# Performance work log

Hardware: AMD Instinct MI355X
Metric: run time of the kernel (lower is better)

The kernel has to match this reference:

```python
import jax, jax.numpy as jnp
import numpy as np

K = 1e-3          # sigmoid temperature from MAPLoss(k=0.001): sigmoid(x) = 1/(1+exp(-x/K))
N, D = 512, 128   # batch of embeddings
NUM_CLASSES = 32
EPS = 1e-8


def setup_inputs() -> dict:
    key = jax.random.key(0)
    k1, k2 = jax.random.split(key)
    return {
        "input": jax.random.normal(k1, (N, D), dtype=jnp.float32),
        "target": jax.random.randint(k2, (N,), 0, NUM_CLASSES, dtype=jnp.int64),
    }


def _offdiag_cols(n):
    # cols[i, j] = j-th column index != i, in increasing order (matches
    # torch sm[~eye].view(n, n-1) row-major off-diagonal extraction)
    idx = jnp.arange(n - 1)[None, :]
    rows = jnp.arange(n)[:, None]
    return idx + (idx >= rows)  # [n, n-1] int


def reference(input, target):
    n = input.shape[0]
    # cosine similarity matrix
    norms = jnp.maximum(jnp.linalg.norm(input, axis=1, keepdims=True), EPS)
    xn = input / norms
    sm = xn @ xn.T  # [n, n]

    cols = _offdiag_cols(n)  # [n, n-1]
    ranking = jnp.take_along_axis(sm, cols, axis=1)  # [n, n-1]
    gt_full = (target[None, :] == target[:, None])    # [n, n] bool
    gt = jnp.take_along_axis(gt_full, cols, axis=1).astype(input.dtype)  # [n, n-1]

    # indicator[i, j, l] = sigmoid((r[i, l] - r[i, j]) / K)   -- O(n^3) cube
    indicator = jax.nn.sigmoid((ranking[:, None, :] - ranking[:, :, None]) / K)

    accumulated_gt = jnp.einsum('il,ijl->ij', gt, indicator)  # [n, n-1]
    denom = indicator.sum(-1) + 0.5                           # [n, n-1]
    prec = accumulated_gt / denom
    ap = jnp.sum(gt * prec, axis=1)    # [n]
    num_positives = gt.sum(-1)         # [n]

    valid = num_positives > 0
    ap_norm = jnp.where(valid, ap / jnp.where(valid, num_positives, 1.0), 0.0)
    n_valid = valid.sum().astype(input.dtype)
    return 1.0 - ap_norm.sum() / n_valid
```

## Files before the change

### kernel.cpp

```cpp
#include <hip/hip_runtime.h>

#define N 512
#define D 128
#define TS 32
#define RS_SCALE 1442.6950408889634f
#define W_INV (1.0f / 18.0f)
#define B_OFF 1530.0f
#define PADV -1600.0f
#define NB 172

static __device__ __forceinline__ float rcp_fast(float x) {
    return __builtin_amdgcn_rcpf(x);
}
static __device__ __forceinline__ float exp2_fast(float x) {
    return __builtin_amdgcn_exp2f(x);
}

__global__ __launch_bounds__(256) void map_sim_kernel(
    const float* __restrict__ x, float* __restrict__ rs,
    int* __restrict__ ticket)
{
    const int bi = blockIdx.x, bj = blockIdx.y, t = threadIdx.x;
    __shared__ float As[TS * D], Bs[TS * D];
    __shared__ float ssA[TS], ssB[TS];
    __shared__ float invA[TS], invB[TS];

    if (bi == 0 && bj == 0 && t == 0) *ticket = 0;

    const int lane = t & 63;
#pragma unroll
    for (int r = 0; r < 4; ++r) {
        int ch = t + 256 * r;
        int row = ch >> 5, c4 = ch & 31;
        int sw = (c4 ^ (row >> 1)) << 2;
        float4 va = *(const float4*)(x + (bi * TS + row) * D + c4 * 4);
        *(float4*)(As + row * D + sw) = va;
        float pa = va.x * va.x + va.y * va.y + va.z * va.z + va.w * va.w;
        float4 vb = *(const float4*)(x + (bj * TS + row) * D + c4 * 4);
        *(float4*)(Bs + row * D + sw) = vb;
        float pb = vb.x * vb.x + vb.y * vb.y + vb.z * vb.z + vb.w * vb.w;
#pragma unroll
        for (int off = 16; off; off >>= 1) {
            pa += __shfl_xor(pa, off);
            pb += __shfl_xor(pb, off);
        }
        if ((lane & 31) == 0) { ssA[row] = pa; ssB[row] = pb; }
    }
    __syncthreads();
    if (t < TS)          invA[t] = rcp_fast(fmaxf(sqrtf(ssA[t]), 1e-8f));
    else if (t < 2 * TS) invB[t - TS] = rcp_fast(fmaxf(sqrtf(ssB[t - TS]), 1e-8f));
    __syncthreads();

    const int tx = t & 15, ty = t >> 4;
    float acc00 = 0.f, acc01 = 0.f, acc10 = 0.f, acc11 = 0.f;
#pragma unroll 4
    for (int k4 = 0; k4 < D / 4; ++k4) {
        float4 a0 = *(const float4*)(As + (2 * ty) * D + ((k4 ^ ty) << 2));
        float4 a1 = *(const float4*)(As + (2 * ty + 1) * D + ((k4 ^ ty) << 2));
        float4 b0 = *(const float4*)(Bs + (2 * tx) * D + ((k4 ^ tx) << 2));
        float4 b1 = *(const float4*)(Bs + (2 * tx + 1) * D + ((k4 ^ tx) << 2));
        acc00 = fmaf(a0.x, b0.x, acc00); acc00 = fmaf(a0.y, b0.y, acc00);
        acc00 = fmaf(a0.z, b0.z, acc00); acc00 = fmaf(a0.w, b0.w, acc00);
        acc01 = fmaf(a0.x, b1.x, acc01); acc01 = fmaf(a0.y, b1.y, acc01);
        acc01 = fmaf(a0.z, b1.z, acc01); acc01 = fmaf(a0.w, b1.w, acc01);
        acc10 = fmaf(a1.x, b0.x, acc10); acc10 = fmaf(a1.y, b0.y, acc10);
        acc10 = fmaf(a1.z, b0.z, acc10); acc10 = fmaf(a1.w, b0.w, acc10);
        acc11 = fmaf(a1.x, b1.x, acc11); acc11 = fmaf(a1.y, b1.y, acc11);
        acc11 = fmaf(a1.z, b1.z, acc11); acc11 = fmaf(a1.w, b1.w, acc11);
    }

    const float sA0 = invA[2 * ty] * RS_SCALE;
    const float sA1 = invA[2 * ty + 1] * RS_SCALE;
    const float sB0 = invB[2 * tx], sB1 = invB[2 * tx + 1];
    const int gr = bi * TS + 2 * ty, gc = bj * TS + 2 * tx;
    *(float2*)(rs + gr * N + gc) =
        make_float2(acc00 * sA0 * sB0, acc01 * sA0 * sB1);
    *(float2*)(rs + (gr + 1) * N + gc) =
        make_float2(acc10 * sA1 * sB0, acc11 * sA1 * sB1);
}

__global__ __launch_bounds__(256) void map_ap_kernel(
    const float* __restrict__ rs, const int* __restrict__ tgt,
    float2* __restrict__ av, int* __restrict__ ticket,
    float* __restrict__ out)
{
    const int i = blockIdx.x, t = threadIdx.x;
    const int lane = t & 63;
    __shared__ int hist[256];
    __shared__ int offs[NB];
    __shared__ int wtot[4];
    __shared__ __align__(16) float2 skv[N];
    __shared__ float red[8];
    __shared__ int amLast;

    hist[t] = 0;
    if (t < NB) offs[t] = 0;
    const int ti = tgt[i];
    float val[2]; int gti[2], q[2];
#pragma unroll
    for (int e = 0; e < 2; ++e) {
        int c = t + 256 * e;
        bool self = (c == i);
        val[e] = self ? PADV : rs[i * N + c];
        gti[e] = (!self && tgt[c] == ti) ? 1 : 0;
        int qq = (int)((val[e] + B_OFF) * W_INV);
        q[e] = max(0, min(NB - 1, qq));
    }
    __syncthreads();
    atomicAdd(&hist[q[0]], (1 << 10) | gti[0]);
    atomicAdd(&hist[q[1]], (1 << 10) | gti[1]);
    __syncthreads();

    int v = hist[t];
#pragma unroll
    for (int off = 1; off < 64; off <<= 1) {
        int u = __shfl_up(v, off);
        if (lane >= off) v += u;
    }
    if (lane == 63) wtot[t >> 6] = v;
    __syncthreads();
    {
        int w = t >> 6, add = 0;
        if (w > 0) add += wtot[0];
        if (w > 1) add += wtot[1];
        if (w > 2) add += wtot[2];
        hist[t] = v + add;
    }
    __syncthreads();

#pragma unroll
    for (int e = 0; e < 2; ++e) {
        int base = (q[e] > 0) ? (hist[q[e] - 1] >> 10) : 0;
        int pos = base + atomicAdd(&offs[q[e]], 1);
        skv[pos] = make_float2(val[e], (float)gti[e]);
    }
    __syncthreads();

    const int totGt = hist[NB - 1] & 1023;
    const float4* skv4 = (const float4*)skv;

    float apAcc = 0.f, npAcc = 0.f;
#pragma unroll
    for (int ri = 0; ri < 2; ++ri) {
        const int p = t + 256 * ri;
        const float2 me = skv[p];
        const float rj = me.x, gtj = me.y;
        int qj = (int)((rj + B_OFF) * W_INV);
        qj = max(0, min(NB - 1, qj));
        const int qlo = __shfl(qj, 0);
        const int qhi = __shfl(qj, 63);
        const int lo = (qlo > 1) ? (hist[qlo - 2] >> 10) : 0;
        const int e1 = min(qhi + 1, NB - 1);
        const int hi = hist[e1] >> 10;

        float dsum = (float)(N - hi);
        float gsum = (float)(totGt - (hist[e1] & 1023));
        int k = lo & ~1;
        for (; k + 2 <= hi; k += 2) {
            float4 kv = skv4[k >> 1];
            float s0 = rcp_fast(1.f + exp2_fast(rj - kv.x));
            float s1 = rcp_fast(1.f + exp2_fast(rj - kv.z));
            dsum += s0 + s1;
            gsum = fmaf(kv.y, s0, gsum);
            gsum = fmaf(kv.w, s1, gsum);
        }
        if (k < hi) {
            float2 kv = skv[k];
            float s = rcp_fast(1.f + exp2_fast(rj - kv.x));
            dsum += s;
            gsum = fmaf(kv.y, s, gsum);
        }
        apAcc += gtj * gsum * rcp_fast(dsum + 0.5f);
        npAcc += gtj;
    }

#pragma unroll
    for (int off = 32; off; off >>= 1) {
        apAcc += __shfl_down(apAcc, off);
        npAcc += __shfl_down(npAcc, off);
    }
    if (lane == 0) { red[(t >> 6) * 2] = apAcc; red[(t >> 6) * 2 + 1] = npAcc; }
    __syncthreads();
    if (t == 0) {
        float A = red[0] + red[2] + red[4] + red[6];
        float P = red[1] + red[3] + red[5] + red[7];
        av[i] = make_float2((P > 0.f) ? (A * rcp_fast(P)) : 0.f,
                            (P > 0.f) ? 1.f : 0.f);
        __threadfence();
        int old = atomicAdd(ticket, 1);
        amLast = (old == (int)gridDim.x - 1) ? 1 : 0;
    }
    __syncthreads();

    if (amLast) {
        __threadfence();
        float2 p0 = av[t], p1 = av[t + 256];
        float a = p0.x + p1.x, vv = p0.y + p1.y;
#pragma unroll
        for (int off = 32; off; off >>= 1) {
            a += __shfl_down(a, off);
            vv += __shfl_down(vv, off);
        }
        if (lane == 0) { red[(t >> 6) * 2] = a; red[(t >> 6) * 2 + 1] = vv; }
        __syncthreads();
        if (t == 0) {
            float A = red[0] + red[2] + red[4] + red[6];
            float V = red[1] + red[3] + red[5] + red[7];
            out[0] = 1.0f - A * rcp_fast(V);
        }
    }
}

extern "C" void kernel_launch(void* const* d_in, const int* in_sizes, int n_in,
                              void* d_out, int out_size, void* d_ws, size_t ws_size,
                              hipStream_t stream) {
    const float* x = (const float*)d_in[0];
    const int* tgt = (const int*)d_in[1];
    float* out = (float*)d_out;

    float* rs = (float*)d_ws;
    float2* av = (float2*)((char*)d_ws + N * N * 4);
    int* ticket = (int*)((char*)d_ws + N * N * 4 + N * 8);

    map_sim_kernel<<<dim3(N / TS, N / TS), 256, 0, stream>>>(x, rs, ticket);
    map_ap_kernel<<<N, 256, 0, stream>>>(rs, tgt, av, ticket, out);
}
```

Baseline: 33.01 us.

## Pack ground-truth flags into bitmask and unroll sigmoid window loop by eight

Replaces the interleaved (value, gt) float2 shared array with a separate float key array and a 512-bit gt bitmask built with atomicOr. The windowed sigmoid loop now handles eight keys per iteration with two float4 loads and one bitmask word, spreading the sums over four independent accumulators to expose ILP. The global loads of rs and tgt are also hoisted ahead of the shared-memory initialisation. This halves shared-memory traffic for the keys, in exchange for extra bit-extract and select instructions, an atomicOr pass during the scatter, and a scalar tail loop that can run longer because the start is aligned down to a multiple of eight.

```diff
diff --git a/kernel.cpp b/kernel.cpp
--- a/kernel.cpp
+++ b/kernel.cpp
@@ -89,20 +89,27 @@
     __shared__ int hist[256];
     __shared__ int offs[NB];
     __shared__ int wtot[4];
-    __shared__ __align__(16) float2 skv[N];
+    __shared__ unsigned gbits[16];
+    __shared__ __align__(16) float skey[N];
     __shared__ float red[8];
     __shared__ int amLast;
 
+    const int ti = tgt[i];
+    const float v0raw = rs[i * N + t];
+    const float v1raw = rs[i * N + t + 256];
+    const int tg0 = tgt[t], tg1 = tgt[t + 256];
+
     hist[t] = 0;
     if (t < NB) offs[t] = 0;
-    const int ti = tgt[i];
+    if (t < 16) gbits[t] = 0u;
+
     float val[2]; int gti[2], q[2];
+    val[0] = (t == i) ? PADV : v0raw;
+    val[1] = (t + 256 == i) ? PADV : v1raw;
+    gti[0] = (t != i && tg0 == ti) ? 1 : 0;
+    gti[1] = (t + 256 != i && tg1 == ti) ? 1 : 0;
 #pragma unroll
     for (int e = 0; e < 2; ++e) {
-        int c = t + 256 * e;
-        bool self = (c == i);
-        val[e] = self ? PADV : rs[i * N + c];
-        gti[e] = (!self && tgt[c] == ti) ? 1 : 0;
         int qq = (int)((val[e] + B_OFF) * W_INV);
         q[e] = max(0, min(NB - 1, qq));
     }
@@ -132,19 +139,20 @@
     for (int e = 0; e < 2; ++e) {
         int base = (q[e] > 0) ? (hist[q[e] - 1] >> 10) : 0;
         int pos = base + atomicAdd(&offs[q[e]], 1);
-        skv[pos] = make_float2(val[e], (float)gti[e]);
+        skey[pos] = val[e];
+        if (gti[e]) atomicOr(&gbits[pos >> 5], 1u << (pos & 31));
     }
     __syncthreads();
 
     const int totGt = hist[NB - 1] & 1023;
-    const float4* skv4 = (const float4*)skv;
+    const float4* sk4 = (const float4*)skey;
 
     float apAcc = 0.f, npAcc = 0.f;
 #pragma unroll
     for (int ri = 0; ri < 2; ++ri) {
         const int p = t + 256 * ri;
-        const float2 me = skv[p];
-        const float rj = me.x, gtj = me.y;
+        const float rj = skey[p];
+        const float gtj = (float)((gbits[p >> 5] >> (p & 31)) & 1u);
         int qj = (int)((rj + B_OFF) * W_INV);
         qj = max(0, min(NB - 1, qj));
         const int qlo = __shfl(qj, 0);
@@ -155,21 +163,40 @@
 
         float dsum = (float)(N - hi);
         float gsum = (float)(totGt - (hist[e1] & 1023));
-        int k = lo & ~1;
-        for (; k + 2 <= hi; k += 2) {
-            float4 kv = skv4[k >> 1];
-            float s0 = rcp_fast(1.f + exp2_fast(rj - kv.x));
-            float s1 = rcp_fast(1.f + exp2_fast(rj - kv.z));
-            dsum += s0 + s1;
-            gsum = fmaf(kv.y, s0, gsum);
-            gsum = fmaf(kv.w, s1, gsum);
-        }
-        if (k < hi) {
-            float2 kv = skv[k];
-            float s = rcp_fast(1.f + exp2_fast(rj - kv.x));
+
+        float d0 = 0.f, d1 = 0.f, d2 = 0.f, d3 = 0.f;
+        float g0 = 0.f, g1 = 0.f, g2 = 0.f, g3 = 0.f;
+        int k = lo & ~7;
+        for (; k + 8 <= hi; k += 8) {
+            float4 ka = sk4[k >> 2];
+            float4 kb = sk4[(k >> 2) + 1];
+            unsigned gw = (gbits[k >> 5] >> (k & 31)) & 0xffu;
+            float s0 = rcp_fast(1.f + exp2_fast(rj - ka.x));
+            float s1 = rcp_fast(1.f + exp2_fast(rj - ka.y));
+            float s2 = rcp_fast(1.f + exp2_fast(rj - ka.z));
+            float s3 = rcp_fast(1.f + exp2_fast(rj - ka.w));
+            float s4 = rcp_fast(1.f + exp2_fast(rj - kb.x));
+            float s5 = rcp_fast(1.f + exp2_fast(rj - kb.y));
+            float s6 = rcp_fast(1.f + exp2_fast(rj - kb.z));
+            float s7 = rcp_fast(1.f + exp2_fast(rj - kb.w));
+            d0 += s0 + s4; d1 += s1 + s5; d2 += s2 + s6; d3 += s3 + s7;
+            g0 += ((gw      ) & 1u) ? s0 : 0.f;
+            g1 += ((gw >> 1u) & 1u) ? s1 : 0.f;
+            g2 += ((gw >> 2u) & 1u) ? s2 : 0.f;
+            g3 += ((gw >> 3u) & 1u) ? s3 : 0.f;
+            g0 += ((gw >> 4u) & 1u) ? s4 : 0.f;
+            g1 += ((gw >> 5u) & 1u) ? s5 : 0.f;
+            g2 += ((gw >> 6u) & 1u) ? s6 : 0.f;
+            g3 += ((gw >> 7u) & 1u) ? s7 : 0.f;
+        }
+        dsum += (d0 + d1) + (d2 + d3);
+        gsum += (g0 + g1) + (g2 + g3);
+        for (; k < hi; ++k) {
+            float s = rcp_fast(1.f + exp2_fast(rj - skey[k]));
             dsum += s;
-            gsum = fmaf(kv.y, s, gsum);
-        }
+            gsum += ((gbits[k >> 5] >> (k & 31)) & 1u) ? s : 0.f;
+        }
+
         apAcc += gtj * gsum * rcp_fast(dsum + 0.5f);
         npAcc += gtj;
     }
```

After: 30.48 us. 7.7% less time.
